# Performance work log

Measured on AMD Instinct MI355X. Metric: run time of the kernel, lower is better.

Reference implementation:

```python
import jax, jax.numpy as jnp
import numpy as np
from jax import lax

SLOPE = 25.0  # snntorch surrogate.fast_sigmoid default slope
NUM_STEPS = 25

@jax.custom_vjp
def spike_fn(x):
    # forward: heaviside(x > 0); backward: fast-sigmoid surrogate grad
    return (x > 0).astype(x.dtype)

def _spike_fwd(x):
    return spike_fn(x), x

def _spike_bwd(x, g):
    return (g / (SLOPE * jnp.abs(x) + 1.0) ** 2,)

spike_fn.defvjp(_spike_fwd, _spike_bwd)


def setup_inputs() -> dict:
    key = jax.random.key(0)
    ks = jax.random.split(key, 6)
    B, NI, NH, NO = 32768, 256, 1024, 1
    x = jax.random.normal(ks[0], (B, NI), dtype=jnp.float32)
    W1 = jax.random.normal(ks[1], (NH, NI), dtype=jnp.float32) / np.sqrt(NI)
    b1 = jax.random.normal(ks[2], (NH,), dtype=jnp.float32) * 0.01
    W2 = jax.random.normal(ks[3], (NO, NH), dtype=jnp.float32) / np.sqrt(NH)
    b2 = jax.random.normal(ks[4], (NO,), dtype=jnp.float32) * 0.01
    beta = jnp.asarray(0.9, dtype=jnp.float32)       # learn_beta=True scalar
    thr = jnp.full((NH,), 1.0, dtype=jnp.float32)    # learn_threshold=True
    return {"x": x, "W1": W1, "b1": b1, "W2": W2, "b2": b2, "beta": beta, "thr": thr}


def reference(x, W1, b1, W2, b2, beta, thr):
    x1 = x @ W1.T + b1                      # [B, NH], constant input each step
    beta_c = jnp.clip(beta, 0.0, 1.0)

    def step(carry, _):
        mem, spk_sum = carry
        reset = spike_fn(mem - thr)         # reset based on previous membrane
        mem_new = beta_c * mem + x1 - reset * thr  # subtract reset mechanism
        spk = spike_fn(mem_new - thr)
        return (mem_new, spk_sum + spk), None

    init = (jnp.zeros_like(x1), jnp.zeros_like(x1))
    (mem, spk_sum), _ = lax.scan(step, init, None, length=NUM_STEPS)
    return spk_sum @ W2.T + b2              # [B, 1]
```

## Files before the change

### kernel.cpp

```cpp
#include <hip/hip_runtime.h>


#define NI 256
#define NH 1024
#define NSTEPS 25
#define BT 128
#define BK 32
#define NTILES (NI / BK)
#define BPS 33
#define RW 40

typedef _Float16 half8 __attribute__((ext_vector_type(8)));
typedef _Float16 half4 __attribute__((ext_vector_type(4)));
typedef float float4v __attribute__((ext_vector_type(4)));

__device__ __forceinline__ unsigned f2k(float f) {
    unsigned u = __float_as_uint(f);
    return (u >> 31) ? ~u : (u | 0x80000000u);
}
__device__ __forceinline__ float k2f(unsigned k) {
    unsigned u = (k & 0x80000000u) ? (k & 0x7FFFFFFFu) : ~k;
    return __uint_as_float(u);
}

__device__ __forceinline__ int lif_count(float x1, float beta, float th) {
    float mem = 0.f;
    float spk = (0.f > th) ? 1.f : 0.f;
    int c = 0;
#pragma unroll
    for (int t = 0; t < NSTEPS; t++) {
        mem = fmaf(spk, -th, fmaf(beta, mem, x1));
        spk = (mem > th) ? 1.f : 0.f;
        c += (mem > th);
    }
    return c;
}

__device__ __forceinline__ void split8(const float* src, half8* hi, half8* lo) {
    float4v a = *(const float4v*)src;
    float4v b = *(const float4v*)(src + 4);
#pragma unroll
    for (int e = 0; e < 4; e++) {
        _Float16 h = (_Float16)a[e];
        (*hi)[e] = h;
        (*lo)[e] = (_Float16)(a[e] - (float)h);
        h = (_Float16)b[e];
        (*hi)[e + 4] = h;
        (*lo)[e + 4] = (_Float16)(b[e] - (float)h);
    }
}

__device__ __forceinline__ void round8(const float* src, half8* hi) {
    float4v a = *(const float4v*)src;
    float4v b = *(const float4v*)(src + 4);
#pragma unroll
    for (int e = 0; e < 4; e++) {
        (*hi)[e]     = (_Float16)a[e];
        (*hi)[e + 4] = (_Float16)b[e];
    }
}


__global__ __launch_bounds__(256) void snn_prep(
    const float* __restrict__ x, const float* __restrict__ W1,
    const float* __restrict__ thr, const float* __restrict__ betap,
    const float* __restrict__ b1, const float* __restrict__ b2,
    float* __restrict__ out, float* __restrict__ bp,
    _Float16* __restrict__ whp, _Float16* __restrict__ wlp,
    _Float16* __restrict__ xhp, int B)
{
    const int tid = threadIdx.x;
    const int XB = B / 8;
    int bid = blockIdx.x;

    if (bid < XB) {
        const int G = bid * 256 + tid;
        const int band = G >> 12;
        const int rem = G & 4095;
        const int kt = rem >> 9;
        const int rem2 = rem & 511;
        const int r8 = rem2 >> 6, quad = (rem2 >> 4) & 3, col = rem2 & 15;
        const float* src = x + (size_t)(band * 128 + r8 * 16 + col) * NI + kt * 32 + quad * 8;
        half8 hi;
        round8(src, &hi);
        ((half8*)xhp)[G] = hi;
        return;
    }
    bid -= XB;
    if (bid < 128) {
        const int G = bid * 256 + tid;
        const int band = G >> 12;
        const int rem = G & 4095;
        const int kt = rem >> 9;
        const int rem2 = rem & 511;
        const int r8 = rem2 >> 6, quad = (rem2 >> 4) & 3, col = rem2 & 15;
        const float* src = W1 + (size_t)(band * 128 + r8 * 16 + col) * NI + kt * 32 + quad * 8;
        half8 hi, lo;
        split8(src, &hi, &lo);
        ((half8*)whp)[G] = hi;
        ((half8*)wlp)[G] = lo;
        return;
    }
    bid -= 128;
    if (bid < 100) {
        const int idx = bid * 256 + tid;
        const int h = idx / NSTEPS;
        const int k = idx % NSTEPS + 1;
        const float th = thr[h];
        const float bj = b1[h];
        float beta = betap[0];
        beta = beta < 0.f ? 0.f : (beta > 1.f ? 1.f : beta);
        unsigned lo = f2k(-3.0e38f), hi = f2k(3.0e38f);
        float res;
        if (lif_count(k2f(hi) + bj, beta, th) < k) {
            res = 3.0e38f;
        } else if (lif_count(k2f(lo) + bj, beta, th) >= k) {
            res = -3.0e38f;
        } else {
#pragma unroll 1
            for (int it = 0; it < 32; it++) {
                unsigned mid = lo + ((hi - lo) >> 1);
                if (lif_count(k2f(mid) + bj, beta, th) >= k) hi = mid; else lo = mid;
            }
            res = k2f(hi);
        }
        bp[h * 32 + (k - 1)] = res;
        return;
    }
    bid -= 100;
    {
        const int i = bid * 256 + tid;
        if (i < B) out[i] = b2[0];
    }
}

__global__ __launch_bounds__(256, 4) void snn_main_fast(
    const _Float16* __restrict__ xhp, const _Float16* __restrict__ whp,
    const _Float16* __restrict__ wlp, const float* __restrict__ W2,
    const float* __restrict__ bp, float* __restrict__ out)
{
    __shared__ float smem[128 * BPS];

    const int tid  = threadIdx.x;
    const int w    = tid >> 6;
    const int lane = tid & 63;
    const int col  = lane & 15;
    const int quad = lane >> 4;
    const int wbb  = (w >> 1) * 64;
    const int whh  = (w & 1) * 64;
    const int bband = blockIdx.x;
    const int hband = blockIdx.y;
    const int b0 = bband * BT;
    const int h0 = hband * BT;
    const int loff = quad * 16 + col;

    const half8* xh = (const half8*)xhp + (size_t)bband * 4096 + (w >> 1) * 256 + loff;
    const half8* wh = (const half8*)whp + (size_t)hband * 4096 + (w & 1) * 256 + loff;
    const half8* wl = (const half8*)wlp + (size_t)hband * 4096 + (w & 1) * 256 + loff;

    float* bpl = smem;
#pragma unroll
    for (int rep = 0; rep < 16; rep++) {
        const int n = tid + 256 * rep;
        const int hl = n >> 5, k = n & 31;
        const float v = bp[(h0 + hl) * 32 + k];
        bpl[hl * BPS + k] = (k < NSTEPS) ? v : 3.0e38f;
    }
    if (tid < BT) bpl[tid * BPS + 32] = W2[h0 + tid];

    float4v acc[4][4];
#pragma unroll
    for (int i = 0; i < 4; i++)
#pragma unroll
        for (int j = 0; j < 4; j++) acc[i][j] = (float4v){0.f, 0.f, 0.f, 0.f};

#pragma unroll 2
    for (int kt = 0; kt < NTILES; kt++) {
        const int gi = kt * 512;
        half8 ah[4], bh[4], bl[4];
#pragma unroll
        for (int i = 0; i < 4; i++) ah[i] = xh[gi + i * 64];
#pragma unroll
        for (int j = 0; j < 4; j++) {
            bh[j] = wh[gi + j * 64];
            bl[j] = wl[gi + j * 64];
        }
#pragma unroll
        for (int j = 0; j < 4; j++)
#pragma unroll
            for (int i = 0; i < 4; i++) {
                acc[i][j] = __builtin_amdgcn_mfma_f32_16x16x32_f16(ah[i], bh[j], acc[i][j], 0, 0, 0);
                acc[i][j] = __builtin_amdgcn_mfma_f32_16x16x32_f16(ah[i], bl[j], acc[i][j], 0, 0, 0);
            }
    }

    __syncthreads();

    float part[16];
#pragma unroll
    for (int e = 0; e < 16; e++) part[e] = 0.f;

#pragma unroll
    for (int j = 0; j < 4; j++) {
        const int hl = whh + 16 * j + col;
        const float* pj = bpl + hl * BPS;
        const float w2 = pj[32];
        const float c16 = pj[15];
        const float c8  = pj[7],  c24 = pj[23];
        const float c4a = pj[3],  c4b = pj[11];
        const float c4c = pj[19], c4d = pj[27];
#pragma unroll
        for (int half = 0; half < 2; half++) {
            float x1[8];
            int mo[8];
#pragma unroll
            for (int e = 0; e < 8; e++) {
                const int ee = e + 8 * half;
                x1[e] = acc[ee >> 2][j][ee & 3];
            }
#pragma unroll
            for (int e = 0; e < 8; e++) {
                const bool g16 = x1[e] >= c16;
                const float cb = g16 ? c24 : c8;
                const bool g8 = x1[e] >= cb;
                const float cc = g16 ? (g8 ? c4d : c4c) : (g8 ? c4b : c4a);
                int m = (g16 ? 16 : 0) + (g8 ? 8 : 0);
                m += (x1[e] >= cc) ? 4 : 0;
                mo[e] = m;
            }
#pragma unroll
            for (int bstep = 2; bstep >= 1; bstep >>= 1) {
#pragma unroll
                for (int e = 0; e < 8; e++) {
                    const float c = pj[mo[e] + bstep - 1];
                    mo[e] += (x1[e] >= c) ? bstep : 0;
                }
            }
#pragma unroll
            for (int e = 0; e < 8; e++)
                part[e + 8 * half] = fmaf((float)mo[e], w2, part[e + 8 * half]);
        }
    }

    __syncthreads();
    float* red = smem;
#pragma unroll
    for (int e = 0; e < 16; e++) {
        const int row = wbb + 16 * (e >> 2) + 4 * quad + (e & 3);
        red[row * 33 + (w & 1) * 16 + col] = part[e];
    }
    __syncthreads();
    if (tid < BT) {
        float s = 0.f;
#pragma unroll
        for (int c2 = 0; c2 < 32; c2++) s += red[tid * 33 + c2];
        atomicAdd(&out[b0 + tid], s);
    }
}


__global__ __launch_bounds__(256) void snn_prep_small(
    const float* __restrict__ thr, const float* __restrict__ betap,
    const float* __restrict__ b2, float* __restrict__ out,
    float* __restrict__ bp, int B)
{
    const int tid = threadIdx.x;
    int bid = blockIdx.x;
    if (bid < 100) {
        const int idx = bid * 256 + tid;
        const int h = idx / NSTEPS;
        const int k = idx % NSTEPS + 1;
        const float th = thr[h];
        float beta = betap[0];
        beta = beta < 0.f ? 0.f : (beta > 1.f ? 1.f : beta);
        unsigned lo = f2k(-3.0e38f), hi = f2k(3.0e38f);
        float res;
        if (lif_count(k2f(hi), beta, th) < k) res = 3.0e38f;
        else if (lif_count(k2f(lo), beta, th) >= k) res = -3.0e38f;
        else {
#pragma unroll 1
            for (int it = 0; it < 32; it++) {
                unsigned mid = lo + ((hi - lo) >> 1);
                if (lif_count(k2f(mid), beta, th) >= k) hi = mid; else lo = mid;
            }
            res = k2f(hi);
        }
        bp[(k - 1) * NH + h] = res;
        return;
    }
    bid -= 100;
    const int i = bid * 256 + tid;
    if (i < B) out[i] = b2[0];
}

__global__ __launch_bounds__(256, 3) void snn_main_fb(
    const float* __restrict__ x, const float* __restrict__ W1,
    const float* __restrict__ b1, const float* __restrict__ W2,
    const float* __restrict__ bp, float* __restrict__ out)
{
    __shared__ __align__(16) _Float16 lds[4 * BT * RW];
    _Float16* xh = lds;
    _Float16* xl = lds + BT * RW;
    _Float16* wh = lds + 2 * BT * RW;
    _Float16* wl = lds + 3 * BT * RW;

    const int tid  = threadIdx.x;
    const int w    = tid >> 6;
    const int lane = tid & 63;
    const int col  = lane & 15;
    const int quad = lane >> 4;
    const int wbb  = (w >> 1) * 64;
    const int whh  = (w & 1) * 64;
    const int b0 = blockIdx.x * BT;
    const int h0 = blockIdx.y * BT;

    float4v acc[4][4];
#pragma unroll
    for (int i = 0; i < 4; i++)
#pragma unroll
        for (int j = 0; j < 4; j++) acc[i][j] = (float4v){0.f, 0.f, 0.f, 0.f};

    const int r0 = tid >> 3;
    const int c4 = tid & 7;
    const float* xrow = x + (size_t)(b0 + r0) * NI + 4 * c4;
    const float* wrow = W1 + (size_t)(h0 + r0) * NI + 4 * c4;

    for (int kt = 0; kt < NTILES; kt++) {
        const int ko = kt * BK;
        float4v vx[4], vw[4];
#pragma unroll
        for (int p = 0; p < 4; p++) {
            vx[p] = *(const float4v*)(xrow + (size_t)(32 * p) * NI + ko);
            vw[p] = *(const float4v*)(wrow + (size_t)(32 * p) * NI + ko);
        }
        __syncthreads();
#pragma unroll
        for (int p = 0; p < 4; p++) {
            const int row = r0 + 32 * p;
            half4 hx, lx, hw, lw;
#pragma unroll
            for (int q = 0; q < 4; q++) {
                float v = vx[p][q];
                _Float16 h = (_Float16)v;
                hx[q] = h;
                lx[q] = (_Float16)(v - (float)h);
                v = vw[p][q];
                h = (_Float16)v;
                hw[q] = h;
                lw[q] = (_Float16)(v - (float)h);
            }
            *(half4*)&xh[row * RW + 4 * c4] = hx;
            *(half4*)&xl[row * RW + 4 * c4] = lx;
            *(half4*)&wh[row * RW + 4 * c4] = hw;
            *(half4*)&wl[row * RW + 4 * c4] = lw;
        }
        __syncthreads();

        half8 ah[4], al[4];
#pragma unroll
        for (int i = 0; i < 4; i++) {
            ah[i] = *(const half8*)&xh[(wbb + 16 * i + col) * RW + 8 * quad];
            al[i] = *(const half8*)&xl[(wbb + 16 * i + col) * RW + 8 * quad];
        }
#pragma unroll
        for (int j = 0; j < 4; j++) {
            half8 bh = *(const half8*)&wh[(whh + 16 * j + col) * RW + 8 * quad];
            half8 bl = *(const half8*)&wl[(whh + 16 * j + col) * RW + 8 * quad];
#pragma unroll
            for (int i = 0; i < 4; i++) {
                acc[i][j] = __builtin_amdgcn_mfma_f32_16x16x32_f16(ah[i], bh, acc[i][j], 0, 0, 0);
                acc[i][j] = __builtin_amdgcn_mfma_f32_16x16x32_f16(ah[i], bl, acc[i][j], 0, 0, 0);
                acc[i][j] = __builtin_amdgcn_mfma_f32_16x16x32_f16(al[i], bh, acc[i][j], 0, 0, 0);
            }
        }
    }

    __syncthreads();
    float* bpl = (float*)lds;
    for (int n = tid; n < NSTEPS * 128; n += 256)
        bpl[n] = bp[(n >> 7) * NH + h0 + (n & 127)];
    __syncthreads();

    float part[16];
#pragma unroll
    for (int e = 0; e < 16; e++) part[e] = 0.f;
#pragma unroll
    for (int j = 0; j < 4; j++) {
        const int hl = whh + 16 * j + col;
        const int h = h0 + hl;
        const float w2 = W2[h];
        const float bj = b1[h];
        float x1[16];
        int cnt[16];
#pragma unroll
        for (int e = 0; e < 16; e++) {
            x1[e] = acc[e >> 2][j][e & 3] + bj;
            cnt[e] = 0;
        }
#pragma unroll
        for (int k = 0; k < NSTEPS; k++) {
            const float c = bpl[k * 128 + hl];
#pragma unroll
            for (int e = 0; e < 16; e++) cnt[e] += (x1[e] >= c) ? 1 : 0;
        }
#pragma unroll
        for (int e = 0; e < 16; e++)
            part[e] = fmaf((float)cnt[e], w2, part[e]);
    }

    __syncthreads();
    float* red = (float*)lds;
#pragma unroll
    for (int e = 0; e < 16; e++) {
        const int row = wbb + 16 * (e >> 2) + 4 * quad + (e & 3);
        red[row * 33 + (w & 1) * 16 + col] = part[e];
    }
    __syncthreads();
    if (tid < BT) {
        float s = 0.f;
#pragma unroll
        for (int c = 0; c < 32; c++) s += red[tid * 33 + c];
        atomicAdd(&out[b0 + tid], s);
    }
}

extern "C" void kernel_launch(void* const* d_in, const int* in_sizes, int n_in,
                              void* d_out, int out_size, void* d_ws, size_t ws_size,
                              hipStream_t stream) {
    const float* x    = (const float*)d_in[0];
    const float* W1   = (const float*)d_in[1];
    const float* b1   = (const float*)d_in[2];
    const float* W2   = (const float*)d_in[3];
    const float* b2   = (const float*)d_in[4];
    const float* beta = (const float*)d_in[5];
    const float* thr  = (const float*)d_in[6];
    float* out = (float*)d_out;

    const int B = in_sizes[0] / NI;

    char* ws = (char*)d_ws;
    float*     bp  = (float*)ws;
    size_t off = (size_t)NH * 32 * 4;
    _Float16* whp = (_Float16*)(ws + off);  off += (size_t)NH * NI * 2;
    _Float16* wlp = (_Float16*)(ws + off);  off += (size_t)NH * NI * 2;
    _Float16* xhp = (_Float16*)(ws + off);  off += (size_t)B * NI * 2;
    const size_t ws_need = off;

    if (ws_size >= ws_need) {
        const int nblk = B / 8 + 128 + 100 + (B + 255) / 256;
        snn_prep<<<nblk, 256, 0, stream>>>(x, W1, thr, beta, b1, b2, out,
                                           bp, whp, wlp, xhp, B);
        dim3 grid(B / BT, NH / BT);
        snn_main_fast<<<grid, 256, 0, stream>>>(xhp, whp, wlp, W2, bp, out);
    } else {
        snn_prep_small<<<100 + (B + 255) / 256, 256, 0, stream>>>(thr, beta, b2, out, bp, B);
        dim3 grid(B / BT, NH / BT);
        snn_main_fb<<<grid, 256, 0, stream>>>(x, W1, b1, W2, bp, out);
    }
}
```

Baseline: 148.6 us.

## Repack per-neuron spike thresholds for vectorized LDS search and float4 tail lookup

The prep kernel now writes each neuron's sorted spike-count thresholds into a 40-float record whose header holds the binary-search pivots and W2, followed by sentinel-padded thresholds. The main kernel copies these records into shared memory with float4 loads and reads the pivots with two vector loads. The last two binary-search levels become one float4 gather plus three compares. This cuts scalar LDS loads and the dependent lookup chain in the epilogue, at the cost of a larger workspace and extra scattered writes in prep.

Result: no change. 146.3 us (-1.5%).

```diff
diff --git a/kernel.cpp b/kernel.cpp
--- a/kernel.cpp
+++ b/kernel.cpp
@@ -8,6 +8,8 @@
 #define BK 32
 #define NTILES (NI / BK)
 #define BPS 33
+#define SROW 44
+#define BPW 40
 #define RW 40
 
 typedef _Float16 half8 __attribute__((ext_vector_type(8)));
@@ -65,6 +67,7 @@
     const float* __restrict__ x, const float* __restrict__ W1,
     const float* __restrict__ thr, const float* __restrict__ betap,
     const float* __restrict__ b1, const float* __restrict__ b2,
+    const float* __restrict__ W2,
     float* __restrict__ out, float* __restrict__ bp,
     _Float16* __restrict__ whp, _Float16* __restrict__ wlp,
     _Float16* __restrict__ xhp, int B)
@@ -124,7 +127,21 @@
             }
             res = k2f(hi);
         }
-        bp[h * 32 + (k - 1)] = res;
+        float* s = bp + (size_t)h * BPW;
+        s[8 + k] = res;
+        if (k == 16) s[0] = res;
+        if (k == 8)  s[1] = res;
+        if (k == 24) s[2] = res;
+        if (k == 4)  s[3] = res;
+        if (k == 12) s[4] = res;
+        if (k == 20) s[5] = res;
+        if (k == 1) {
+            s[6] = 3.0e38f;
+            s[7] = W2[h];
+            s[8] = -3.0e38f;
+#pragma unroll
+            for (int i = 26; i < 32; i++) s[8 + i] = 3.0e38f;
+        }
         return;
     }
     bid -= 100;
@@ -139,7 +156,7 @@
     const _Float16* __restrict__ wlp, const float* __restrict__ W2,
     const float* __restrict__ bp, float* __restrict__ out)
 {
-    __shared__ float smem[128 * BPS];
+    __shared__ __align__(16) float smem[128 * SROW];
 
     const int tid  = threadIdx.x;
     const int w    = tid >> 6;
@@ -158,15 +175,16 @@
     const half8* wh = (const half8*)whp + (size_t)hband * 4096 + (w & 1) * 256 + loff;
     const half8* wl = (const half8*)wlp + (size_t)hband * 4096 + (w & 1) * 256 + loff;
 
-    float* bpl = smem;
-#pragma unroll
-    for (int rep = 0; rep < 16; rep++) {
-        const int n = tid + 256 * rep;
-        const int hl = n >> 5, k = n & 31;
-        const float v = bp[(h0 + hl) * 32 + k];
-        bpl[hl * BPS + k] = (k < NSTEPS) ? v : 3.0e38f;
-    }
-    if (tid < BT) bpl[tid * BPS + 32] = W2[h0 + tid];
+    {
+        const float* bpg = bp + (size_t)h0 * BPW;
+#pragma unroll
+        for (int r = 0; r < 5; r++) {
+            const int f = tid + 256 * r;
+            const int row = f / 10, kq = f % 10;
+            const float4v v = *(const float4v*)(bpg + (size_t)f * 4);
+            *(float4v*)(smem + row * SROW + kq * 4) = v;
+        }
+    }
 
     float4v acc[4][4];
 #pragma unroll
@@ -203,12 +221,12 @@
 #pragma unroll
     for (int j = 0; j < 4; j++) {
         const int hl = whh + 16 * j + col;
-        const float* pj = bpl + hl * BPS;
-        const float w2 = pj[32];
-        const float c16 = pj[15];
-        const float c8  = pj[7],  c24 = pj[23];
-        const float c4a = pj[3],  c4b = pj[11];
-        const float c4c = pj[19], c4d = pj[27];
+        const float* pj = smem + hl * SROW;
+        const float4v p0 = *(const float4v*)(pj);
+        const float4v p1 = *(const float4v*)(pj + 4);
+        const float c16 = p0[0], c8 = p0[1], c24 = p0[2];
+        const float c4a = p0[3], c4b = p1[0], c4c = p1[1], c4d = p1[2];
+        const float w2 = p1[3];
 #pragma unroll
         for (int half = 0; half < 2; half++) {
             float x1[8];
@@ -228,17 +246,18 @@
                 m += (x1[e] >= cc) ? 4 : 0;
                 mo[e] = m;
             }
-#pragma unroll
-            for (int bstep = 2; bstep >= 1; bstep >>= 1) {
-#pragma unroll
-                for (int e = 0; e < 8; e++) {
-                    const float c = pj[mo[e] + bstep - 1];
-                    mo[e] += (x1[e] >= c) ? bstep : 0;
-                }
-            }
+            float4v q[8];
 #pragma unroll
             for (int e = 0; e < 8; e++)
-                part[e + 8 * half] = fmaf((float)mo[e], w2, part[e + 8 * half]);
+                q[e] = *(const float4v*)(pj + 8 + mo[e]);
+#pragma unroll
+            for (int e = 0; e < 8; e++) {
+                int m = mo[e];
+                m += (x1[e] >= q[e][1]) ? 1 : 0;
+                m += (x1[e] >= q[e][2]) ? 1 : 0;
+                m += (x1[e] >= q[e][3]) ? 1 : 0;
+                part[e + 8 * half] = fmaf((float)m, w2, part[e + 8 * half]);
+            }
         }
     }
 
@@ -247,13 +266,13 @@
 #pragma unroll
     for (int e = 0; e < 16; e++) {
         const int row = wbb + 16 * (e >> 2) + 4 * quad + (e & 3);
-        red[row * 33 + (w & 1) * 16 + col] = part[e];
+        red[row * BPS + (w & 1) * 16 + col] = part[e];
     }
     __syncthreads();
     if (tid < BT) {
         float s = 0.f;
 #pragma unroll
-        for (int c2 = 0; c2 < 32; c2++) s += red[tid * 33 + c2];
+        for (int c2 = 0; c2 < 32; c2++) s += red[tid * BPS + c2];
         atomicAdd(&out[b0 + tid], s);
     }
 }
@@ -440,7 +459,7 @@
 
     char* ws = (char*)d_ws;
     float*     bp  = (float*)ws;
-    size_t off = (size_t)NH * 32 * 4;
+    size_t off = (size_t)NH * BPW * 4;
     _Float16* whp = (_Float16*)(ws + off);  off += (size_t)NH * NI * 2;
     _Float16* wlp = (_Float16*)(ws + off);  off += (size_t)NH * NI * 2;
     _Float16* xhp = (_Float16*)(ws + off);  off += (size_t)B * NI * 2;
@@ -448,7 +467,7 @@
 
     if (ws_size >= ws_need) {
         const int nblk = B / 8 + 128 + 100 + (B + 255) / 256;
-        snn_prep<<<nblk, 256, 0, stream>>>(x, W1, thr, beta, b1, b2, out,
+        snn_prep<<<nblk, 256, 0, stream>>>(x, W1, thr, beta, b1, b2, W2, out,
                                            bp, whp, wlp, xhp, B);
         dim3 grid(B / BT, NH / BT);
         snn_main_fast<<<grid, 256, 0, stream>>>(xhp, whp, wlp, W2, bp, out);
```
